# Kernel optimization log

Measured on AMD Instinct MI355X. Metric: run time of the kernel, lower is better.

The kernel has to match this reference:

```python
import jax, jax.numpy as jnp
import numpy as np

N_GEN = 6
DIM = 1 << N_GEN  # 64
B, F = 256, 128
EPS = 1e-6


def _build_algebra():
    # Blades as bitmasks over N_GEN generators, canonical grade-then-lex order.
    blades = sorted(range(DIM), key=lambda b: (bin(b).count("1"), b))
    index = {b: i for i, b in enumerate(blades)}
    grades = np.array([bin(b).count("1") for b in blades], dtype=np.int64)
    cls = (grades % 4).astype(np.int32)  # quaternion-type class of each blade

    def swap_sign(a, b):
        s = 0
        a >>= 1
        while a:
            s += bin(a & b).count("1")
            a >>= 1
        return -1.0 if (s & 1) else 1.0

    # cayley[i, j, k] = coefficient of e_j in e_i * e_k (Euclidean metric, +1 squares)
    cayley = np.zeros((DIM, DIM, DIM), dtype=np.float32)
    for bi in range(DIM):
        for bk in range(DIM):
            cayley[index[bi], index[bi ^ bk], index[bk]] = swap_sign(bi, bk)

    # qt_geometric_product_paths: which (class_i, class_j, class_k) triples are nonzero
    paths = np.zeros((4, 4, 4), dtype=bool)
    i_, j_, k_ = np.nonzero(cayley)
    paths[cls[i_], cls[j_], cls[k_]] = True
    return cayley, cls, np.argwhere(paths).astype(np.int32)  # paths.sum() == 32


def setup_inputs() -> dict:
    cayley, cls, pidx = _build_algebra()
    P = pidx.shape[0]
    key = jax.random.key(0)
    k1, k2, k3 = jax.random.split(key, 3)
    x = jax.random.normal(k1, (B, F, DIM), jnp.float32)
    # reset_parameters: std = 1/sqrt(algebra.dim_generators + 1)
    w_gp = jax.random.normal(k2, (F, P), jnp.float32) / np.sqrt(N_GEN + 1)
    w_lin = jax.random.normal(k3, (F, F, 4), jnp.float32) / np.sqrt(F)
    b_lin = jnp.zeros((F,), jnp.float32)
    a_norm = jnp.zeros((F, 4), jnp.float32)  # normalization_init = 0
    return {"x": x, "w_gp": w_gp, "w_lin": w_lin, "b_lin": b_lin,
            "a_norm": a_norm, "cayley": jnp.asarray(cayley),
            "cls": jnp.asarray(cls), "path_idx": jnp.asarray(pidx)}


def reference(x, w_gp, w_lin, b_lin, a_norm, cayley, cls, path_idx):
    # --- QTLinear: per-QT-class channel mixing (weight shared within each class) ---
    w_lin_full = w_lin[:, :, cls]                          # [F_out, F_in, D]
    xr = jnp.einsum('bmi,nmi->bni', x, w_lin_full)         # [B, F, D]
    xr = xr.at[..., 0].add(b_lin)                          # bias on scalar blade only

    # --- QTNormalization: sigmoid-gated per-class norm, interpolated toward 1 ---
    sq = jnp.moveaxis(xr * xr, -1, 0)                      # [D, B, F]
    norms4 = jnp.sqrt(jax.ops.segment_sum(sq, cls, num_segments=4))  # [4, B, F]
    norms4 = jnp.moveaxis(norms4, 0, -1)                   # [B, F, 4]
    gated = jax.nn.sigmoid(a_norm) * (norms4 - 1.0) + 1.0  # [B, F, 4]
    xr = xr / (gated[..., cls] + EPS)                      # broadcast class norm to blades

    # --- _get_weight: scatter path weights into [F,4,4,4], expand to [F,D,D,D] ---
    # (scatter + repeat_interleave + permutation collapses to a class-index gather)
    F_ = w_gp.shape[0]
    full4 = jnp.zeros((F_, 4, 4, 4), x.dtype).at[
        :, path_idx[:, 0], path_idx[:, 1], path_idx[:, 2]].set(w_gp)
    w_full = full4[:, cls[:, None, None], cls[None, :, None], cls[None, None, :]]  # [F,D,D,D]
    weight = cayley[None] * w_full

    # --- weighted geometric product ---
    return jnp.einsum('bni,nijk,bnk->bnj', x, weight, xr)
```

## Files before the change

### kernel.cpp

```cpp
#include <hip/hip_runtime.h>
#include <hip/hip_bf16.h>

namespace alg {
constexpr int pc(int v) { int c = 0; while (v) { c += v & 1; v >>= 1; } return c; }
constexpr int swap_sign_i(int a, int b) {
  int s = 0; a >>= 1;
  while (a) { s += pc(a & b); a >>= 1; }
  return (s & 1) ? -1 : 1;
}
struct Tables {
  int blade[64]; int index[64]; int cls[64];
  int itab[64][64]; int sgn[64][64]; int ct[64][64];
  constexpr Tables() : blade{}, index{}, cls{}, itab{}, sgn{}, ct{} {
    int pos = 0;
    for (int g = 0; g <= 6; ++g)
      for (int b = 0; b < 64; ++b)
        if (pc(b) == g) { blade[pos] = b; index[b] = pos; ++pos; }
    for (int i = 0; i < 64; ++i) cls[i] = pc(blade[i]) & 3;
    for (int J = 0; J < 64; ++J)
      for (int K = 0; K < 64; ++K) {
        int bj = blade[J], bk = blade[K], bi = bj ^ bk;
        int I = index[bi];
        itab[J][K] = I;
        sgn[J][K] = swap_sign_i(bi, bk);
        ct[J][K] = cls[I] * 16 + cls[J] * 4 + cls[K];
      }
  }
};
constexpr Tables T{};
}

__device__ __forceinline__ float rfl(float v) {
  return __uint_as_float(__builtin_amdgcn_readfirstlane(__float_as_uint(v)));
}

__global__ __launch_bounds__(256) void kprep(
    const float* __restrict__ x, const float* __restrict__ wlin,
    const float* __restrict__ wgp, const int* __restrict__ pidx, int P,
    float* __restrict__ xT, float* __restrict__ Wt, float* __restrict__ g) {
  int bid = blockIdx.x;
  if (bid < 512) {
    __shared__ float tile[64 * 65];
    int m = bid >> 2, bc = (bid & 3) << 6;
    int lane = threadIdx.x & 63, row = threadIdx.x >> 6;
#pragma unroll
    for (int p = 0; p < 16; ++p) {
      int b = p * 4 + row;
      tile[lane * 65 + b] = x[(bc + b) * 8192 + m * 64 + lane];
    }
    __syncthreads();
#pragma unroll
    for (int p = 0; p < 16; ++p) {
      int il = p * 4 + row;
      xT[il * 32768 + m * 256 + bc + lane] = tile[il * 65 + lane];
    }
  } else if (bid < 768) {
    int id = (bid - 512) * 256 + threadIdx.x;
    int n = id & 127, m = (id >> 7) & 127, c = id >> 14;
    Wt[c * 16384 + m * 128 + n] = wlin[n * 512 + m * 4 + c];
  } else {
    int id = (bid - 768) * 256 + threadIdx.x;
    int n = id >> 6, t = id & 63;
    int ti = t >> 4, tj = (t >> 2) & 3, tk = t & 3;
    float v = 0.f;
    for (int p = 0; p < P; ++p)
      if (pidx[p * 3] == ti && pidx[p * 3 + 1] == tj && pidx[p * 3 + 2] == tk)
        v = wgp[n * P + p];
    g[n * 64 + t] = v;
  }
}

__global__ __launch_bounds__(512) void klin(
    const float* __restrict__ xT, const float* __restrict__ Wt,
    const float* __restrict__ blin, float* __restrict__ xrT) {
  __shared__ float xs[128 * 64];
  int bid = blockIdx.x;
  int i = bid >> 2;
  int bc = (bid & 3) << 6;
  int ci = alg::T.cls[i];
  int t = threadIdx.x;
  {
    int b = t & 63, m0 = t >> 6;
    const float* src = xT + i * 32768 + bc + b;
#pragma unroll
    for (int r = 0; r < 16; ++r) {
      int m = m0 * 16 + r;
      xs[m * 64 + b] = src[m * 256];
    }
  }
  __syncthreads();

  int w = __builtin_amdgcn_readfirstlane(t >> 6);
  int lane = t & 63;
  const float4* wp4 = (const float4*)Wt + ci * 4096 + w * 4;
  float acc[16];
#pragma unroll
  for (int q = 0; q < 16; ++q) acc[q] = 0.f;

#pragma unroll 4
  for (int m = 0; m < 128; ++m) {
    float xv = xs[m * 64 + lane];
#pragma unroll
    for (int q = 0; q < 4; ++q) {
      float4 wv = wp4[m * 32 + q];
      acc[q * 4 + 0] = fmaf(xv, wv.x, acc[q * 4 + 0]);
      acc[q * 4 + 1] = fmaf(xv, wv.y, acc[q * 4 + 1]);
      acc[q * 4 + 2] = fmaf(xv, wv.z, acc[q * 4 + 2]);
      acc[q * 4 + 3] = fmaf(xv, wv.w, acc[q * 4 + 3]);
    }
  }
  if (i == 0) {
#pragma unroll
    for (int q = 0; q < 16; ++q) acc[q] += blin[w * 16 + q];
  }
#pragma unroll
  for (int q = 0; q < 16; ++q)
    xrT[(w * 16 + q) * 16384 + i * 256 + bc + lane] = acc[q];
}

template <int JW>
__device__ __forceinline__ void prod_body(
    const float* __restrict__ xv, const float* __restrict__ rv,
    const float* __restrict__ gl, float* __restrict__ out,
    float* __restrict__ ot, int n, int bc, int lane) {
  float acc[16];
#pragma unroll
  for (int jj = 0; jj < 16; ++jj) acc[jj] = 0.f;
#pragma unroll
  for (int k = 0; k < 64; ++k) {
#pragma unroll
    for (int jj = 0; jj < 16; ++jj) {
      const int j = JW * 16 + jj;
      const int ii = alg::T.itab[j][k];
      const int tt = alg::T.ct[j][k];
      float t = xv[ii] * rv[k];
      acc[jj] = fmaf(alg::T.sgn[j][k] > 0 ? gl[tt] : -gl[tt], t, acc[jj]);
    }
  }
#pragma unroll
  for (int jj = 0; jj < 16; ++jj) ot[jj * 68 + lane] = acc[jj];
  __builtin_amdgcn_s_waitcnt(0);
#pragma unroll
  for (int p = 0; p < 16; ++p) {
    int j = lane & 15, br = p * 4 + (lane >> 4);
    out[(bc + br) * 8192 + n * 64 + JW * 16 + j] = ot[j * 68 + br];
  }
}

__global__ __launch_bounds__(256, 2) void kprod(
    const float* __restrict__ xT, const float* __restrict__ xr,
    const float* __restrict__ g, const float* __restrict__ an,
    float* __restrict__ out) {
  __shared__ float smem[8192];
  float* xs = smem;
  float* rs = smem + 4096;
  int bid = blockIdx.x;
  int n = bid >> 2;
  int bc = (bid & 3) << 6;
  int t = threadIdx.x;
  int w = __builtin_amdgcn_readfirstlane(t >> 6);
  int lane = t & 63;

  {
    int b = t & 63, i0 = t >> 6;
    const float* sx = xT + n * 256 + bc + b;
    const float* sr = xr + n * 16384 + bc + b;
#pragma unroll
    for (int r = 0; r < 16; ++r) {
      int i = i0 * 16 + r;
      xs[i * 64 + b] = sx[i * 32768];
      rs[i * 64 + b] = sr[i * 256];
    }
  }
  __syncthreads();

  float xv[64], rv[64];
#pragma unroll
  for (int i = 0; i < 64; ++i) xv[i] = xs[i * 64 + lane];
#pragma unroll
  for (int i = 0; i < 64; ++i) rv[i] = rs[i * 64 + lane];

  float gl[64];
#pragma unroll
  for (int q = 0; q < 64; ++q) gl[q] = rfl(g[n * 64 + q]);

  float s[4] = {0.f, 0.f, 0.f, 0.f};
#pragma unroll
  for (int i = 0; i < 64; ++i) {
    const int c = alg::T.cls[i];
    s[c] = fmaf(rv[i], rv[i], s[c]);
  }
  float r[4];
#pragma unroll
  for (int c = 0; c < 4; ++c) {
    float a = rfl(an[n * 4 + c]);
    float sig = 1.f / (1.f + __expf(-a));
    float gate = sig * (sqrtf(s[c]) - 1.f) + 1.f;
    r[c] = 1.f / (gate + 1e-6f);
  }
#pragma unroll
  for (int i = 0; i < 64; ++i) rv[i] *= r[alg::T.cls[i]];

  __syncthreads();
  float* ot = smem + w * 1088;

  switch (w) {
    case 0: prod_body<0>(xv, rv, gl, out, ot, n, bc, lane); break;
    case 1: prod_body<1>(xv, rv, gl, out, ot, n, bc, lane); break;
    case 2: prod_body<2>(xv, rv, gl, out, ot, n, bc, lane); break;
    case 3: prod_body<3>(xv, rv, gl, out, ot, n, bc, lane); break;
  }
}

extern "C" void kernel_launch(void* const* d_in, const int* in_sizes, int n_in,
                              void* d_out, int out_size, void* d_ws, size_t ws_size,
                              hipStream_t stream) {
  (void)n_in; (void)out_size; (void)ws_size;
  const float* x    = (const float*)d_in[0];
  const float* wgp  = (const float*)d_in[1];
  const float* wlin = (const float*)d_in[2];
  const float* blin = (const float*)d_in[3];
  const float* an   = (const float*)d_in[4];
  const int*   pidx = (const int*)d_in[7];
  int P = in_sizes[7] / 3;

  float* ws  = (float*)d_ws;
  float* xT  = ws;
  float* xrT = ws + 2097152;
  float* Wt  = ws + 4194304;
  float* g   = ws + 4259840;

  kprep<<<800, 256, 0, stream>>>(x, wlin, wgp, pidx, P, xT, Wt, g);
  klin<<<256, 512, 0, stream>>>(xT, Wt, blin, xrT);
  kprod<<<512, 256, 0, stream>>>(xT, xrT, g, an, (float*)d_out);
}
```

Measured before the change: 109.7 us.

## Fuse prep, linear and product kernels into one persistent kernel with grid barriers

Replaces the three launches (prep, linear mixing, geometric product) with a single 256-block kernel that uses atomic-counter grid barriers between stages, plus a memset to reset the counters. The product stage now reads x directly in its original layout through a padded shared tile instead of the transposed copy. The aim is to remove launch gaps and inter-kernel drain. In exchange the product stage runs with half as many blocks, two sub-tiles per 512-thread block, which may cut occupancy. The spin barrier also relies on all 256 blocks being resident at the same time.

```diff
diff --git a/kernel.cpp b/kernel.cpp
--- a/kernel.cpp
+++ b/kernel.cpp
@@ -1,5 +1,4 @@
 #include <hip/hip_runtime.h>
-#include <hip/hip_bf16.h>
 
 namespace alg {
 constexpr int pc(int v) { int c = 0; while (v) { c += v & 1; v >>= 1; } return c; }
@@ -34,88 +33,15 @@
   return __uint_as_float(__builtin_amdgcn_readfirstlane(__float_as_uint(v)));
 }
 
-__global__ __launch_bounds__(256) void kprep(
-    const float* __restrict__ x, const float* __restrict__ wlin,
-    const float* __restrict__ wgp, const int* __restrict__ pidx, int P,
-    float* __restrict__ xT, float* __restrict__ Wt, float* __restrict__ g) {
-  int bid = blockIdx.x;
-  if (bid < 512) {
-    __shared__ float tile[64 * 65];
-    int m = bid >> 2, bc = (bid & 3) << 6;
-    int lane = threadIdx.x & 63, row = threadIdx.x >> 6;
-#pragma unroll
-    for (int p = 0; p < 16; ++p) {
-      int b = p * 4 + row;
-      tile[lane * 65 + b] = x[(bc + b) * 8192 + m * 64 + lane];
-    }
-    __syncthreads();
-#pragma unroll
-    for (int p = 0; p < 16; ++p) {
-      int il = p * 4 + row;
-      xT[il * 32768 + m * 256 + bc + lane] = tile[il * 65 + lane];
-    }
-  } else if (bid < 768) {
-    int id = (bid - 512) * 256 + threadIdx.x;
-    int n = id & 127, m = (id >> 7) & 127, c = id >> 14;
-    Wt[c * 16384 + m * 128 + n] = wlin[n * 512 + m * 4 + c];
-  } else {
-    int id = (bid - 768) * 256 + threadIdx.x;
-    int n = id >> 6, t = id & 63;
-    int ti = t >> 4, tj = (t >> 2) & 3, tk = t & 3;
-    float v = 0.f;
-    for (int p = 0; p < P; ++p)
-      if (pidx[p * 3] == ti && pidx[p * 3 + 1] == tj && pidx[p * 3 + 2] == tk)
-        v = wgp[n * P + p];
-    g[n * 64 + t] = v;
-  }
-}
-
-__global__ __launch_bounds__(512) void klin(
-    const float* __restrict__ xT, const float* __restrict__ Wt,
-    const float* __restrict__ blin, float* __restrict__ xrT) {
-  __shared__ float xs[128 * 64];
-  int bid = blockIdx.x;
-  int i = bid >> 2;
-  int bc = (bid & 3) << 6;
-  int ci = alg::T.cls[i];
-  int t = threadIdx.x;
-  {
-    int b = t & 63, m0 = t >> 6;
-    const float* src = xT + i * 32768 + bc + b;
-#pragma unroll
-    for (int r = 0; r < 16; ++r) {
-      int m = m0 * 16 + r;
-      xs[m * 64 + b] = src[m * 256];
-    }
-  }
+__device__ __forceinline__ void gbar(unsigned int* c, unsigned int target) {
   __syncthreads();
-
-  int w = __builtin_amdgcn_readfirstlane(t >> 6);
-  int lane = t & 63;
-  const float4* wp4 = (const float4*)Wt + ci * 4096 + w * 4;
-  float acc[16];
-#pragma unroll
-  for (int q = 0; q < 16; ++q) acc[q] = 0.f;
-
-#pragma unroll 4
-  for (int m = 0; m < 128; ++m) {
-    float xv = xs[m * 64 + lane];
-#pragma unroll
-    for (int q = 0; q < 4; ++q) {
-      float4 wv = wp4[m * 32 + q];
-      acc[q * 4 + 0] = fmaf(xv, wv.x, acc[q * 4 + 0]);
-      acc[q * 4 + 1] = fmaf(xv, wv.y, acc[q * 4 + 1]);
-      acc[q * 4 + 2] = fmaf(xv, wv.z, acc[q * 4 + 2]);
-      acc[q * 4 + 3] = fmaf(xv, wv.w, acc[q * 4 + 3]);
-    }
-  }
-  if (i == 0) {
-#pragma unroll
-    for (int q = 0; q < 16; ++q) acc[q] += blin[w * 16 + q];
-  }
-#pragma unroll
-  for (int q = 0; q < 16; ++q)
-    xrT[(w * 16 + q) * 16384 + i * 256 + bc + lane] = acc[q];
+  __threadfence();
+  if (threadIdx.x == 0) {
+    atomicAdd(c, 1u);
+    while (atomicAdd(c, 0u) < target) __builtin_amdgcn_s_sleep(1);
+  }
+  __syncthreads();
+  __threadfence();
 }
 
 template <int JW>
@@ -147,68 +73,164 @@
   }
 }
 
-__global__ __launch_bounds__(256, 2) void kprod(
-    const float* __restrict__ xT, const float* __restrict__ xr,
-    const float* __restrict__ g, const float* __restrict__ an,
-    float* __restrict__ out) {
-  __shared__ float smem[8192];
-  float* xs = smem;
-  float* rs = smem + 4096;
+__global__ __launch_bounds__(512, 2) void kfused(
+    const float* __restrict__ x, const float* __restrict__ wlin,
+    const float* __restrict__ wgp, const int* __restrict__ pidx, int P,
+    const float* __restrict__ blin, const float* __restrict__ an,
+    float* __restrict__ xT, float* __restrict__ xrT,
+    float* __restrict__ Wt, float* __restrict__ g,
+    unsigned int* __restrict__ bar, float* __restrict__ out) {
+  __shared__ float smem[16768];
   int bid = blockIdx.x;
-  int n = bid >> 2;
-  int bc = (bid & 3) << 6;
   int t = threadIdx.x;
-  int w = __builtin_amdgcn_readfirstlane(t >> 6);
-  int lane = t & 63;
 
   {
-    int b = t & 63, i0 = t >> 6;
-    const float* sx = xT + n * 256 + bc + b;
-    const float* sr = xr + n * 16384 + bc + b;
-#pragma unroll
-    for (int r = 0; r < 16; ++r) {
-      int i = i0 * 16 + r;
-      xs[i * 64 + b] = sx[i * 32768];
-      rs[i * 64 + b] = sr[i * 256];
-    }
-  }
-  __syncthreads();
-
-  float xv[64], rv[64];
-#pragma unroll
-  for (int i = 0; i < 64; ++i) xv[i] = xs[i * 64 + lane];
-#pragma unroll
-  for (int i = 0; i < 64; ++i) rv[i] = rs[i * 64 + lane];
-
-  float gl[64];
-#pragma unroll
-  for (int q = 0; q < 64; ++q) gl[q] = rfl(g[n * 64 + q]);
-
-  float s[4] = {0.f, 0.f, 0.f, 0.f};
-#pragma unroll
-  for (int i = 0; i < 64; ++i) {
-    const int c = alg::T.cls[i];
-    s[c] = fmaf(rv[i], rv[i], s[c]);
-  }
-  float r[4];
-#pragma unroll
-  for (int c = 0; c < 4; ++c) {
-    float a = rfl(an[n * 4 + c]);
-    float sig = 1.f / (1.f + __expf(-a));
-    float gate = sig * (sqrtf(s[c]) - 1.f) + 1.f;
-    r[c] = 1.f / (gate + 1e-6f);
-  }
-#pragma unroll
-  for (int i = 0; i < 64; ++i) rv[i] *= r[alg::T.cls[i]];
-
-  __syncthreads();
-  float* ot = smem + w * 1088;
-
-  switch (w) {
-    case 0: prod_body<0>(xv, rv, gl, out, ot, n, bc, lane); break;
-    case 1: prod_body<1>(xv, rv, gl, out, ot, n, bc, lane); break;
-    case 2: prod_body<2>(xv, rv, gl, out, ot, n, bc, lane); break;
-    case 3: prod_body<3>(xv, rv, gl, out, ot, n, bc, lane); break;
+    int s = t >> 8, tl = t & 255;
+    int u = bid * 2 + s;
+    float* tile = smem + s * 4160;
+    int m = u >> 2, bc = (u & 3) << 6;
+    int lane = tl & 63, row = tl >> 6;
+#pragma unroll
+    for (int p = 0; p < 16; ++p) {
+      int b = p * 4 + row;
+      tile[lane * 65 + b] = x[(bc + b) * 8192 + m * 64 + lane];
+    }
+    __syncthreads();
+#pragma unroll
+    for (int p = 0; p < 16; ++p) {
+      int il = p * 4 + row;
+      xT[il * 32768 + m * 256 + bc + lane] = tile[il * 65 + lane];
+    }
+    if (t < 256) {
+      int id = bid * 256 + t;
+      int n = id & 127, mm = (id >> 7) & 127, c = id >> 14;
+      Wt[c * 16384 + mm * 128 + n] = wlin[n * 512 + mm * 4 + c];
+    }
+    if (t < 32) {
+      int id = bid * 32 + t;
+      int n = id >> 6, tt = id & 63;
+      int ti = tt >> 4, tj = (tt >> 2) & 3, tk = tt & 3;
+      float v = 0.f;
+      for (int p = 0; p < P; ++p)
+        if (pidx[p * 3] == ti && pidx[p * 3 + 1] == tj && pidx[p * 3 + 2] == tk)
+          v = wgp[n * P + p];
+      g[n * 64 + tt] = v;
+    }
+  }
+  gbar(bar, 256);
+
+  {
+    float* xs = smem;
+    int i = bid >> 2;
+    int bc = (bid & 3) << 6;
+    int ci = alg::T.cls[i];
+    {
+      int b = t & 63, m0 = t >> 6;
+      const float* src = xT + i * 32768 + bc + b;
+#pragma unroll
+      for (int r = 0; r < 16; ++r) {
+        int m = m0 * 16 + r;
+        xs[m * 64 + b] = src[m * 256];
+      }
+    }
+    __syncthreads();
+
+    int w = __builtin_amdgcn_readfirstlane(t >> 6);
+    int lane = t & 63;
+    const float4* wp4 = (const float4*)Wt + ci * 4096 + w * 4;
+    float acc[16];
+#pragma unroll
+    for (int q = 0; q < 16; ++q) acc[q] = 0.f;
+
+#pragma unroll 4
+    for (int m = 0; m < 128; ++m) {
+      float xv = xs[m * 64 + lane];
+#pragma unroll
+      for (int q = 0; q < 4; ++q) {
+        float4 wv = wp4[m * 32 + q];
+        acc[q * 4 + 0] = fmaf(xv, wv.x, acc[q * 4 + 0]);
+        acc[q * 4 + 1] = fmaf(xv, wv.y, acc[q * 4 + 1]);
+        acc[q * 4 + 2] = fmaf(xv, wv.z, acc[q * 4 + 2]);
+        acc[q * 4 + 3] = fmaf(xv, wv.w, acc[q * 4 + 3]);
+      }
+    }
+    if (i == 0) {
+#pragma unroll
+      for (int q = 0; q < 16; ++q) acc[q] += blin[w * 16 + q];
+    }
+#pragma unroll
+    for (int q = 0; q < 16; ++q)
+      xrT[(w * 16 + q) * 16384 + i * 256 + bc + lane] = acc[q];
+  }
+  gbar(bar + 32, 256);
+
+  {
+    int s = t >> 8, tl = t & 255;
+    int u = bid * 2 + s;
+    int n = u >> 2;
+    int bc = (u & 3) << 6;
+    float* base = smem + s * 8384;
+    float* xs2 = base;
+    float* rs = base + 4160;
+    int w = __builtin_amdgcn_readfirstlane((tl >> 6) & 3);
+    int lane = tl & 63;
+
+    {
+      int i = tl & 63, b0 = tl >> 6;
+      const float* sx = x + n * 64 + i;
+#pragma unroll
+      for (int r = 0; r < 16; ++r) {
+        int b = r * 4 + b0;
+        xs2[b * 65 + i] = sx[(bc + b) * 8192];
+      }
+    }
+    {
+      int b = tl & 63, i0 = tl >> 6;
+      const float* sr = xrT + n * 16384 + bc + b;
+#pragma unroll
+      for (int r = 0; r < 16; ++r) {
+        int i = i0 * 16 + r;
+        rs[b * 65 + i] = sr[i * 256];
+      }
+    }
+    __syncthreads();
+
+    float xv[64], rv[64];
+#pragma unroll
+    for (int i = 0; i < 64; ++i) xv[i] = xs2[lane * 65 + i];
+#pragma unroll
+    for (int i = 0; i < 64; ++i) rv[i] = rs[lane * 65 + i];
+
+    float gl[64];
+#pragma unroll
+    for (int q = 0; q < 64; ++q) gl[q] = rfl(g[n * 64 + q]);
+
+    float sq[4] = {0.f, 0.f, 0.f, 0.f};
+#pragma unroll
+    for (int i = 0; i < 64; ++i) {
+      const int c = alg::T.cls[i];
+      sq[c] = fmaf(rv[i], rv[i], sq[c]);
+    }
+    float r[4];
+#pragma unroll
+    for (int c = 0; c < 4; ++c) {
+      float a = rfl(an[n * 4 + c]);
+      float sig = 1.f / (1.f + __expf(-a));
+      float gate = sig * (sqrtf(sq[c]) - 1.f) + 1.f;
+      r[c] = 1.f / (gate + 1e-6f);
+    }
+#pragma unroll
+    for (int i = 0; i < 64; ++i) rv[i] *= r[alg::T.cls[i]];
+
+    __syncthreads();
+    float* ot = base + w * 1088;
+
+    switch (w) {
+      case 0: prod_body<0>(xv, rv, gl, out, ot, n, bc, lane); break;
+      case 1: prod_body<1>(xv, rv, gl, out, ot, n, bc, lane); break;
+      case 2: prod_body<2>(xv, rv, gl, out, ot, n, bc, lane); break;
+      case 3: prod_body<3>(xv, rv, gl, out, ot, n, bc, lane); break;
+    }
   }
 }
 
@@ -229,8 +251,9 @@
   float* xrT = ws + 2097152;
   float* Wt  = ws + 4194304;
   float* g   = ws + 4259840;
-
-  kprep<<<800, 256, 0, stream>>>(x, wlin, wgp, pidx, P, xT, Wt, g);
-  klin<<<256, 512, 0, stream>>>(xT, Wt, blin, xrT);
-  kprod<<<512, 256, 0, stream>>>(xT, xrT, g, an, (float*)d_out);
-}
+  unsigned int* bar = (unsigned int*)(ws + 4268032);
+
+  hipMemsetAsync(bar, 0, 256, stream);
+  kfused<<<256, 512, 0, stream>>>(x, wlin, wgp, pidx, P, blin, an, xT, xrT,
+                                  Wt, g, bar, (float*)d_out);
+}
```

Result: slower. 265.8 us (+142.2%).
